# Performance work log

Hardware: AMD Instinct MI355X
Metric: run time of the kernel (lower is better)

Reference implementation:

```python
import jax, jax.numpy as jnp
import numpy as np

H, CH = 4, 16          # heads, hidden_features // heads
SLOPE = 0.2            # leaky_relu negative slope


def gat(x, W, a_src, a_dst):
    # x: (B, N, C); W: (hidden, C); a_src/a_dst: (H, CH)
    B, N, _ = x.shape
    h = (x @ W.T).reshape(B, N, H, CH)
    a1 = jnp.einsum('bnhc,hc->bnh', h, a_src)   # att_src scores
    a2 = jnp.einsum('bnhc,hc->bnh', h, a_dst)   # att_dst scores
    # torch: a1.unsqueeze(1) + a2.unsqueeze(2) -> (B, N, N, H)
    e = a1[:, None, :, :] + a2[:, :, None, :]
    e = jnp.transpose(e, (0, 3, 1, 2))          # (B, H, N, N)
    e = jnp.where(e >= 0, e, SLOPE * e)         # leaky_relu
    return jax.nn.softmax(e, axis=2)            # softmax over dim=2 as in torch


def pool(x, W1, b1, W2, b2):
    # diff-pool assignment: (B, N, K), then x' = S^T x -> (B, K, C)
    s = jax.nn.softmax(jax.nn.relu(x @ W1.T + b1) @ W2.T + b2, axis=-1)
    return jnp.einsum('bnk,bnc->bkc', s, x)


def fuse(att0, atts, lefts, rights):
    out = att0
    for a, l, r in zip(atts, lefts, rights):
        # left (H,J0,K) @ att (B,H,K,K) @ right (H,K,J0), broadcast over batch
        out = out + jnp.einsum('hjk,bhkl,hlm->bhjm', l, a, r)
    return out


def setup_inputs() -> dict:
    key = jax.random.key(0)
    ks = iter(jax.random.split(key, 40))
    n = lambda shape, s=0.1: jax.random.normal(next(ks), shape, dtype=jnp.float32) * s
    inp = {
        'src': n((64, 64, 64, 25), 1.0),
        'gat_lin': n((6, 64, 64)), 'gat_asrc': n((6, 4, 16)), 'gat_adst': n((6, 4, 16)),
        'sp0_W1': n((64, 64)), 'sp0_b1': jnp.zeros((64,), jnp.float32),
        'sp0_W2': n((12, 64)), 'sp0_b2': jnp.zeros((12,), jnp.float32),
        'sp1_W1': n((64, 64)), 'sp1_b1': jnp.zeros((64,), jnp.float32),
        'sp1_W2': n((5, 64)), 'sp1_b2': jnp.zeros((5,), jnp.float32),
        'tp0_W1': n((64, 64)), 'tp0_b1': jnp.zeros((64,), jnp.float32),
        'tp0_W2': n((32, 64)), 'tp0_b2': jnp.zeros((32,), jnp.float32),
        'tp1_W1': n((64, 64)), 'tp1_b1': jnp.zeros((64,), jnp.float32),
        'tp1_W2': n((12, 64)), 'tp1_b2': jnp.zeros((12,), jnp.float32),
        'sl0': n((4, 25, 12)), 'sr0': n((4, 12, 25)),
        'sl1': n((4, 25, 5)), 'sr1': n((4, 5, 25)),
        'tl0': n((4, 64, 32)), 'tr0': n((4, 32, 64)),
        'tl1': n((4, 64, 12)), 'tr1': n((4, 12, 64)),
    }
    return inp


def reference(src, gat_lin, gat_asrc, gat_adst,
              sp0_W1, sp0_b1, sp0_W2, sp0_b2, sp1_W1, sp1_b1, sp1_W2, sp1_b2,
              tp0_W1, tp0_b1, tp0_W2, tp0_b2, tp1_W1, tp1_b1, tp1_W2, tp1_b2,
              sl0, sr0, sl1, sr1, tl0, tr0, tl1, tr1):
    B, C, T, J = src.shape
    # ---- spatial branch: attention over joints per (batch, frame) ----
    xs = jnp.transpose(src, (0, 2, 3, 1)).reshape(B * T, J, C)
    a_s0 = gat(xs, gat_lin[0], gat_asrc[0], gat_adst[0])            # (BT,H,25,25)
    xs1 = pool(xs, sp0_W1, sp0_b1, sp0_W2, sp0_b2)                  # (BT,12,C)
    a_s1 = gat(xs1, gat_lin[1], gat_asrc[1], gat_adst[1])           # (BT,H,12,12)
    xs2 = pool(xs1, sp1_W1, sp1_b1, sp1_W2, sp1_b2)                 # (BT,5,C)
    a_s2 = gat(xs2, gat_lin[2], gat_asrc[2], gat_adst[2])           # (BT,H,5,5)
    s_fused = fuse(a_s0, [a_s1, a_s2], [sl0, sl1], [sr0, sr1])
    # ---- temporal branch: attention over frames per (batch, joint) ----
    xt = jnp.transpose(src, (0, 3, 2, 1)).reshape(B * J, T, C)
    a_t0 = gat(xt, gat_lin[3], gat_asrc[3], gat_adst[3])            # (BJ,H,64,64)
    xt1 = pool(xt, tp0_W1, tp0_b1, tp0_W2, tp0_b2)                  # (BJ,32,C)
    a_t1 = gat(xt1, gat_lin[4], gat_asrc[4], gat_adst[4])
    xt2 = pool(xt1, tp1_W1, tp1_b1, tp1_W2, tp1_b2)                 # (BJ,12,C)
    a_t2 = gat(xt2, gat_lin[5], gat_asrc[5], gat_adst[5])
    t_fused = fuse(a_t0, [a_t1, a_t2], [tl0, tl1], [tr0, tr1])
    return (s_fused.reshape(B, T, H, J, J), t_fused.reshape(B, J, H, T, T))
```

## Files before the change

### kernel.cpp

```cpp
#include <hip/hip_runtime.h>

#define DEVINL __device__ __forceinline__

DEVINL float leaky(float v) { return v >= 0.f ? v : 0.2f * v; }

typedef float v4f __attribute__((ext_vector_type(4)));

DEVINL void nt_store4(float* p, float4 v) {
    v4f q = {v.x, v.y, v.z, v.w};
    __builtin_nontemporal_store(q, (v4f*)p);
}

__global__ void wprep_kernel(const float* __restrict__ lin,
                             const float* __restrict__ asrc,
                             const float* __restrict__ adst,
                             float* __restrict__ w_out) {
    int idx = blockIdx.x * blockDim.x + threadIdx.x;
    if (idx >= 6 * 4 * 64) return;
    int c = idx & 63;
    int h = (idx >> 6) & 3;
    int k = idx >> 8;
    const float* L = lin + k * 64 * 64;
    float s1 = 0.f, s2 = 0.f;
    for (int e = 0; e < 16; ++e) {
        float w = L[(h * 16 + e) * 64 + c];
        s1 += w * asrc[(k * 4 + h) * 16 + e];
        s2 += w * adst[(k * 4 + h) * 16 + e];
    }
    w_out[(k * 2 + 0) * 256 + h * 64 + c] = s1;
    w_out[(k * 2 + 1) * 256 + h * 64 + c] = s2;
}

__global__ void wtrans_kernel(const float* __restrict__ s0, const float* __restrict__ s1,
                              const float* __restrict__ t0, const float* __restrict__ t1,
                              const float* __restrict__ s0w2, const float* __restrict__ s1w2,
                              const float* __restrict__ t0w2, const float* __restrict__ t1w2,
                              float* __restrict__ o) {
    int idx = blockIdx.x * 256 + threadIdx.x;
    if (idx < 16384) {
        int m = idx >> 12, r = idx & 4095, c = r >> 6, d = r & 63;
        const float* src = (m == 0) ? s0 : (m == 1) ? s1 : (m == 2) ? t0 : t1;
        o[idx] = src[d * 64 + c];
    } else if (idx < 16384 + 768) {
        int j = idx - 16384, c = j / 12, k = j - 12 * c;
        o[idx] = s0w2[k * 64 + c];
    } else if (idx < 17152 + 512) {
        int j = idx - 17152, c = j >> 3, k = j & 7;
        o[idx] = (k < 5) ? s1w2[k * 64 + c] : 0.f;
    } else if (idx < 17664 + 2048) {
        int j = idx - 17664, c = j >> 5, k = j & 31;
        o[idx] = t0w2[k * 64 + c];
    } else if (idx < 19712 + 768) {
        int j = idx - 19712, c = j / 12, k = j - 12 * c;
        o[idx] = t1w2[k * 64 + c];
    }
}

__global__ void xs_kernel(const float* __restrict__ src, float* __restrict__ xs) {
    int g = blockIdx.x;
    int b = g >> 6, t = g & 63;
    __shared__ float tile[64][26];
    const float* sp = src + b * 102400 + t * 25;
    for (int idx = threadIdx.x; idx < 64 * 25; idx += blockDim.x) {
        int c = idx / 25, j = idx - c * 25;
        tile[c][j] = sp[c * 1600 + j];
    }
    __syncthreads();
    float* op = xs + g * 25 * 64;
    for (int idx = threadIdx.x; idx < 25 * 64; idx += blockDim.x) {
        int j = idx >> 6, c = idx & 63;
        op[idx] = tile[c][j];
    }
}

__global__ void xt_kernel(const float* __restrict__ src, float* __restrict__ xt) {
    int g = blockIdx.x;
    int b = g / 25, j = g - b * 25;
    __shared__ float tile[64][65];
    const float* sp = src + b * 102400 + j;
    for (int idx = threadIdx.x; idx < 64 * 64; idx += blockDim.x) {
        int c = idx >> 6, t = idx & 63;
        tile[c][t] = sp[c * 1600 + t * 25];
    }
    __syncthreads();
    float* op = xt + g * 64 * 64;
    for (int idx = threadIdx.x; idx < 64 * 64; idx += blockDim.x) {
        int t = idx >> 6, c = idx & 63;
        op[idx] = tile[c][t];
    }
}

template <int N>
__global__ __launch_bounds__(256) void gat_kernel(
    const float* __restrict__ x,
    const float* __restrict__ w,
    float* __restrict__ att) {
    int g = blockIdx.x;
    const int tid = threadIdx.x;
    __shared__ float xlT[64][N + 1];
    __shared__ float wl[512];
    __shared__ float a1s[4 * N], a2s[4 * N];
    __shared__ float mxs[4];
    __shared__ float mjs[4 * N], invs[4 * N];
    const float* xp = x + (size_t)g * N * 64;
    for (int idx = tid; idx < N * 64; idx += 256) {
        int n = idx >> 6, c = idx & 63;
        xlT[c][n] = xp[idx];
    }
    for (int idx = tid; idx < 512; idx += 256) wl[idx] = w[idx];
    __syncthreads();
    for (int idx = tid; idx < 8 * N; idx += 256) {
        int n = idx % N;
        int hh = (idx / N) & 3;
        int sd = idx / (4 * N);
        const float* wp = wl + sd * 256 + hh * 64;
        float acc = 0.f;
        #pragma unroll 8
        for (int c = 0; c < 64; ++c) acc += xlT[c][n] * wp[c];
        (sd == 0 ? a1s : a2s)[hh * N + n] = acc;
    }
    __syncthreads();
    if (tid < 4) {
        float m = -1e30f;
        for (int i = 0; i < N; ++i) m = fmaxf(m, a2s[tid * N + i]);
        mxs[tid] = m;
    }
    __syncthreads();
    for (int idx = tid; idx < 4 * N; idx += 256) {
        int hh = idx / N;
        float aj = a1s[idx];
        float mj = leaky(aj + mxs[hh]);
        float ssum = 0.f;
        for (int i = 0; i < N; ++i) ssum += __expf(leaky(aj + a2s[hh * N + i]) - mj);
        mjs[idx] = mj;
        invs[idx] = 1.f / ssum;
    }
    __syncthreads();
    float* ob = att + (size_t)g * 4 * N * N;
    if constexpr ((N % 4) == 0) {
        constexpr int NF4 = N / 4;
        for (int idx = tid; idx < 4 * N * NF4; idx += 256) {
            int row = idx / NF4;
            int j0 = (idx - row * NF4) * 4;
            int hh = row / N;
            float4 q1 = *(const float4*)&a1s[hh * N + j0];
            float4 qm = *(const float4*)&mjs[hh * N + j0];
            float4 qv = *(const float4*)&invs[hh * N + j0];
            float a2i = a2s[row];
            float a1v[4] = {q1.x, q1.y, q1.z, q1.w};
            float mv[4] = {qm.x, qm.y, qm.z, qm.w};
            float iv[4] = {qv.x, qv.y, qv.z, qv.w};
            float r[4];
            #pragma unroll
            for (int c = 0; c < 4; ++c) {
                float e = a1v[c] + a2i;
                e = e >= 0.f ? e : 0.2f * e;
                r[c] = __expf(e - mv[c]) * iv[c];
            }
            *(float4*)&ob[row * N + j0] = make_float4(r[0], r[1], r[2], r[3]);
        }
    } else {
        for (int idx = tid; idx < 4 * N * N; idx += 256) {
            int hh = idx / (N * N), rem = idx - hh * N * N;
            int i = rem / N, j = rem - i * N;
            float e = a1s[hh * N + j] + a2s[hh * N + i];
            e = e >= 0.f ? e : 0.2f * e;
            ob[idx] = __expf(e - mjs[hh * N + j]) * invs[hh * N + j];
        }
    }
}

template <int N, int K, int KP>
__global__ __launch_bounds__(256, 3) void pool_kernel(
    const float* __restrict__ x,
    const float* __restrict__ W1T,
    const float* __restrict__ b1,
    const float* __restrict__ W2T,
    const float* __restrict__ b2,
    float* __restrict__ xo) {
    constexpr int NP = (N + 3) & ~3;
    constexpr int LDN = NP + 1;
    __shared__ float xlT[64 * LDN];
    __shared__ float yT[64 * LDN];
    __shared__ float sT[KP * LDN];
    const int g = blockIdx.x, tid = threadIdx.x;
    const float* xp = x + (size_t)g * N * 64;
    for (int i4 = tid; i4 < N * 16; i4 += 256) {
        int n = i4 >> 4, c0 = (i4 & 15) << 2;
        float4 v = ((const float4*)xp)[i4];
        xlT[(c0 + 0) * LDN + n] = v.x;
        xlT[(c0 + 1) * LDN + n] = v.y;
        xlT[(c0 + 2) * LDN + n] = v.z;
        xlT[(c0 + 3) * LDN + n] = v.w;
    }
    if constexpr (NP > N) {
        for (int i = tid; i < 64 * (NP - N); i += 256) {
            int c = i / (NP - N), n = N + i % (NP - N);
            xlT[c * LDN + n] = 0.f;
        }
    }
    __syncthreads();
    constexpr int T1 = (NP / 4) * 16;
    if (tid < T1) {
        int d0 = (tid & 15) << 2, n0 = (tid >> 4) << 2;
        float acc[4][4] = {};
        #pragma unroll 4
        for (int c = 0; c < 64; ++c) {
            float4 w4 = *(const float4*)(W1T + c * 64 + d0);
            float wv[4] = {w4.x, w4.y, w4.z, w4.w};
            float xv[4];
            #pragma unroll
            for (int r = 0; r < 4; ++r) xv[r] = xlT[c * LDN + n0 + r];
            #pragma unroll
            for (int r = 0; r < 4; ++r)
                #pragma unroll
                for (int cc = 0; cc < 4; ++cc) acc[r][cc] += xv[r] * wv[cc];
        }
        float4 b4 = *(const float4*)(b1 + d0);
        float bb[4] = {b4.x, b4.y, b4.z, b4.w};
        #pragma unroll
        for (int r = 0; r < 4; ++r)
            #pragma unroll
            for (int cc = 0; cc < 4; ++cc)
                yT[(d0 + cc) * LDN + n0 + r] = fmaxf(acc[r][cc] + bb[cc], 0.f);
    }
    __syncthreads();
    constexpr int KG4 = KP / 4;
    constexpr int T2 = (NP / 4) * KG4;
    if (tid < T2) {
        int k0 = (tid % KG4) << 2, n0 = (tid / KG4) << 2;
        float acc[4][4] = {};
        #pragma unroll 4
        for (int d = 0; d < 64; ++d) {
            float4 w4 = *(const float4*)(W2T + d * KP + k0);
            float wv[4] = {w4.x, w4.y, w4.z, w4.w};
            float yv[4];
            #pragma unroll
            for (int r = 0; r < 4; ++r) yv[r] = yT[d * LDN + n0 + r];
            #pragma unroll
            for (int r = 0; r < 4; ++r)
                #pragma unroll
                for (int cc = 0; cc < 4; ++cc) acc[r][cc] += yv[r] * wv[cc];
        }
        #pragma unroll
        for (int cc = 0; cc < 4; ++cc) {
            int k = k0 + cc;
            float bb = (k < K) ? b2[k] : 0.f;
            #pragma unroll
            for (int r = 0; r < 4; ++r)
                sT[k * LDN + n0 + r] = (k < K) ? (acc[r][cc] + bb) : -1e30f;
        }
    }
    __syncthreads();
    if (tid < NP) {
        float m = -1e30f;
        #pragma unroll
        for (int k = 0; k < KP; ++k) m = fmaxf(m, sT[k * LDN + tid]);
        float sum = 0.f;
        float e[KP];
        #pragma unroll
        for (int k = 0; k < KP; ++k) { e[k] = __expf(sT[k * LDN + tid] - m); sum += e[k]; }
        float inv = 1.f / sum;
        #pragma unroll
        for (int k = 0; k < KP; ++k) sT[k * LDN + tid] = e[k] * inv;
    }
    __syncthreads();
    constexpr int KG2 = (K + 1) / 2;
    constexpr int T3 = KG2 * 16;
    if (tid < T3) {
        int k0 = (tid % KG2) * 2, c0 = (tid / KG2) * 4;
        float acc0[4] = {}, acc1[4] = {};
        #pragma unroll 4
        for (int n = 0; n < N; ++n) {
            float sv0 = sT[k0 * LDN + n];
            float sv1 = sT[(k0 + 1) * LDN + n];
            float xv[4];
            #pragma unroll
            for (int j = 0; j < 4; ++j) xv[j] = xlT[(c0 + j) * LDN + n];
            #pragma unroll
            for (int j = 0; j < 4; ++j) { acc0[j] += sv0 * xv[j]; acc1[j] += sv1 * xv[j]; }
        }
        float* op = xo + (size_t)g * K * 64;
        *(float4*)&op[k0 * 64 + c0] = make_float4(acc0[0], acc0[1], acc0[2], acc0[3]);
        if (k0 + 1 < K)
            *(float4*)&op[(k0 + 1) * 64 + c0] = make_float4(acc1[0], acc1[1], acc1[2], acc1[3]);
    }
}

__global__ __launch_bounds__(256, 5) void gatfuse_t(
    const float* __restrict__ x,
    const float* __restrict__ w,
    const float* __restrict__ A1g,
    const float* __restrict__ L1,
    const float* __restrict__ R1,
    const float* __restrict__ A2g,
    const float* __restrict__ L2,
    const float* __restrict__ R2,
    float* __restrict__ out)
{
    const int bid = blockIdx.x;
    const int g = (bid & 7) | ((bid >> 5) << 3);
    const int h = (bid >> 3) & 3;
    const int tid = threadIdx.x;
    __shared__ float t1T[32 * 64];
    __shared__ float r1l[32 * 64];
    __shared__ float t2T[12 * 64];
    __shared__ float r2l[12 * 64];
    __shared__ float A1T[32 * 36];
    __shared__ float A2T[12 * 13];
    __shared__ float a1s[64], a2s[64], mjs[64], invs[64];

    if (tid < 128) {
        int t = tid & 63, sd = tid >> 6;
        const float4* xr = (const float4*)(x + (size_t)g * 4096 + t * 64);
        const float* wv = w + sd * 256 + h * 64;
        float acc = 0.f;
        #pragma unroll
        for (int q = 0; q < 16; ++q) {
            float4 xv = xr[q];
            acc += xv.x * wv[q * 4] + xv.y * wv[q * 4 + 1] +
                   xv.z * wv[q * 4 + 2] + xv.w * wv[q * 4 + 3];
        }
        (sd == 0 ? a1s : a2s)[t] = acc;
    } else {
        int u = tid - 128;
        const float* a1p = A1g + (size_t)(g * 4 + h) * 1024;
        #pragma unroll
        for (int q = 0; q < 8; ++q) {
            int idx = q * 128 + u;
            A1T[(idx & 31) * 36 + (idx >> 5)] = a1p[idx];
        }
        const float* a2p = A2g + (size_t)(g * 4 + h) * 144;
        for (int idx = u; idx < 144; idx += 128) {
            int k = idx / 12, l = idx - k * 12;
            A2T[l * 13 + k] = a2p[idx];
        }
        const float4* r1p = (const float4*)(R1 + h * 2048);
        #pragma unroll
        for (int q = 0; q < 4; ++q) ((float4*)r1l)[q * 128 + u] = r1p[q * 128 + u];
        const float4* r2p = (const float4*)(R2 + h * 768);
        for (int idx = u; idx < 192; idx += 128) ((float4*)r2l)[idx] = r2p[idx];
    }
    __syncthreads();

    if (tid < 64) {
        float mx = a2s[0];
        for (int i = 1; i < 64; ++i) mx = fmaxf(mx, a2s[i]);
        float aj = a1s[tid];
        float mj = leaky(aj + mx);
        float ssum = 0.f;
        for (int i = 0; i < 64; ++i) ssum += __expf(leaky(aj + a2s[i]) - mj);
        mjs[tid] = mj;
        invs[tid] = 1.f / ssum;
    }
    {
        int j = tid & 63, l0 = (tid >> 6) * 8;
        float lj[32];
        const float4* lp = (const float4*)(L1 + (h * 64 + j) * 32);
        #pragma unroll
        for (int q = 0; q < 8; ++q) {
            float4 v = lp[q];
            lj[q * 4] = v.x; lj[q * 4 + 1] = v.y; lj[q * 4 + 2] = v.z; lj[q * 4 + 3] = v.w;
        }
        for (int l = l0; l < l0 + 8; ++l) {
            const float* ar = &A1T[l * 36];
            float acc = 0.f;
            #pragma unroll
            for (int k = 0; k < 32; k += 4) {
                float4 av = *(const float4*)&ar[k];
                acc += lj[k] * av.x + lj[k + 1] * av.y + lj[k + 2] * av.z + lj[k + 3] * av.w;
            }
            t1T[l * 64 + j] = acc;
        }
    }
    {
        int j = tid & 63, lb = (tid >> 6) * 3;
        float lj2[12];
        const float* lp2 = L2 + (h * 64 + j) * 12;
        #pragma unroll
        for (int k = 0; k < 12; ++k) lj2[k] = lp2[k];
        for (int l = lb; l < lb + 3; ++l) {
            const float* ar = &A2T[l * 13];
            float acc = 0.f;
            #pragma unroll
            for (int k = 0; k < 12; ++k) acc += lj2[k] * ar[k];
            t2T[l * 64 + j] = acc;
        }
    }
    __syncthreads();

    const int i0 = (tid >> 4) << 2, m0 = (tid & 15) << 2;
    float acc[4][4];
    {
        float4 q1 = *(const float4*)&a1s[m0];
        float4 qm = *(const float4*)&mjs[m0];
        float4 qv = *(const float4*)&invs[m0];
        float4 q2 = *(const float4*)&a2s[i0];
        float am[4] = {q1.x, q1.y, q1.z, q1.w};
        float mv[4] = {qm.x, qm.y, qm.z, qm.w};
        float iv[4] = {qv.x, qv.y, qv.z, qv.w};
        float ai[4] = {q2.x, q2.y, q2.z, q2.w};
        #pragma unroll
        for (int r = 0; r < 4; ++r)
            #pragma unroll
            for (int c = 0; c < 4; ++c) {
                float e = am[c] + ai[r];
                e = e >= 0.f ? e : 0.2f * e;
                acc[r][c] = __expf(e - mv[c]) * iv[c];
            }
    }
    #pragma unroll 8
    for (int l = 0; l < 32; ++l) {
        float4 t4 = *(const float4*)&t1T[l * 64 + i0];
        float4 r4 = *(const float4*)&r1l[l * 64 + m0];
        float tv[4] = {t4.x, t4.y, t4.z, t4.w};
        float rv[4] = {r4.x, r4.y, r4.z, r4.w};
        #pragma unroll
        for (int r = 0; r < 4; ++r)
            #pragma unroll
            for (int c = 0; c < 4; ++c) acc[r][c] += tv[r] * rv[c];
    }
    #pragma unroll 4
    for (int l = 0; l < 12; ++l) {
        float4 t4 = *(const float4*)&t2T[l * 64 + i0];
        float4 r4 = *(const float4*)&r2l[l * 64 + m0];
        float tv[4] = {t4.x, t4.y, t4.z, t4.w};
        float rv[4] = {r4.x, r4.y, r4.z, r4.w};
        #pragma unroll
        for (int r = 0; r < 4; ++r)
            #pragma unroll
            for (int c = 0; c < 4; ++c) acc[r][c] += tv[r] * rv[c];
    }
    float* op = out + (size_t)(g * 4 + h) * 4096;
    #pragma unroll
    for (int r = 0; r < 4; ++r)
        nt_store4(&op[(i0 + r) * 64 + m0],
                  make_float4(acc[r][0], acc[r][1], acc[r][2], acc[r][3]));
}

__global__ __launch_bounds__(256) void gatfuse_s(
    const float* __restrict__ x,
    const float* __restrict__ w,
    const float* __restrict__ A1g,
    const float* __restrict__ L1,
    const float* __restrict__ R1,
    const float* __restrict__ A2g,
    const float* __restrict__ L2,
    const float* __restrict__ R2,
    float* __restrict__ out)
{
    const int g = blockIdx.x;
    const int tid = threadIdx.x;
    const int h = tid >> 6, t = tid & 63;
    __shared__ float xl[25 * 68];
    __shared__ float A1T[4][12 * 12];
    __shared__ float A2T[4][5 * 5];
    __shared__ float t1l[4][25 * 12];
    __shared__ float t2l[4][25 * 5];
    __shared__ float r1l[4][12 * 25];
    __shared__ float r2l[4][5 * 25];
    __shared__ float a1s[4][25], a2s[4][25], mjs[4][32], invs[4][32];

    const float* xp = x + (size_t)g * 1600;
    for (int idx = tid; idx < 1600; idx += 256) {
        int n = idx >> 6, c = idx & 63;
        xl[n * 68 + c] = xp[idx];
    }
    const float* a1p = A1g + (size_t)(g * 4 + h) * 144;
    for (int idx = t; idx < 144; idx += 64) {
        int k = idx / 12, l = idx - k * 12;
        A1T[h][l * 12 + k] = a1p[idx];
    }
    const float* a2p = A2g + (size_t)(g * 4 + h) * 25;
    if (t < 25) {
        int k = t / 5, l = t - 5 * (t / 5);
        A2T[h][l * 5 + k] = a2p[t];
    }
    for (int idx = t; idx < 300; idx += 64) r1l[h][idx] = R1[h * 300 + idx];
    for (int idx = t; idx < 125; idx += 64) r2l[h][idx] = R2[h * 125 + idx];
    __syncthreads();

    if (t < 25) {
        const float* ws_ = w + h * 64;
        const float* wd_ = w + 256 + h * 64;
        const float* xr = &xl[t * 68];
        float s1 = 0.f, s2 = 0.f;
        #pragma unroll
        for (int c = 0; c < 64; c += 4) {
            float4 xv = *(const float4*)&xr[c];
            s1 += xv.x * ws_[c] + xv.y * ws_[c + 1] + xv.z * ws_[c + 2] + xv.w * ws_[c + 3];
            s2 += xv.x * wd_[c] + xv.y * wd_[c + 1] + xv.z * wd_[c + 2] + xv.w * wd_[c + 3];
        }
        a1s[h][t] = s1;
        a2s[h][t] = s2;
    }
    __syncthreads();

    if (t < 25) {
        float mx = a2s[h][0];
        for (int i = 1; i < 25; ++i) mx = fmaxf(mx, a2s[h][i]);
        float aj = a1s[h][t];
        float mj = leaky(aj + mx);
        float ssum = 0.f;
        for (int i = 0; i < 25; ++i) ssum += __expf(leaky(aj + a2s[h][i]) - mj);
        mjs[h][t] = mj;
        invs[h][t] = 1.f / ssum;
        float lj[12];
        const float* lp = L1 + (h * 25 + t) * 12;
        #pragma unroll
        for (int k = 0; k < 12; ++k) lj[k] = lp[k];
        #pragma unroll
        for (int l = 0; l < 12; ++l) {
            const float* ar = &A1T[h][l * 12];
            float acc = 0.f;
            #pragma unroll
            for (int k = 0; k < 12; ++k) acc += lj[k] * ar[k];
            t1l[h][t * 12 + l] = acc;
        }
        float lj2[5];
        const float* lp2 = L2 + (h * 25 + t) * 5;
        #pragma unroll
        for (int k = 0; k < 5; ++k) lj2[k] = lp2[k];
        #pragma unroll
        for (int l = 0; l < 5; ++l) {
            const float* ar = &A2T[h][l * 5];
            float acc = 0.f;
            #pragma unroll
            for (int k = 0; k < 5; ++k) acc += lj2[k] * ar[k];
            t2l[h][t * 5 + l] = acc;
        }
    }
    __syncthreads();

    float* op = out + (size_t)(g * 4 + h) * 625;
    for (int idx = t; idx < 625; idx += 64) {
        int i = idx / 25, m = idx - i * 25;
        float e = a1s[h][m] + a2s[h][i];
        e = e >= 0.f ? e : 0.2f * e;
        float val = __expf(e - mjs[h][m]) * invs[h][m];
        const float* t1r = &t1l[h][i * 12];
        const float* r1c = &r1l[h][m];
        #pragma unroll
        for (int l = 0; l < 12; ++l) val += t1r[l] * r1c[l * 25];
        const float* t2r = &t2l[h][i * 5];
        const float* r2c = &r2l[h][m];
        #pragma unroll
        for (int l = 0; l < 5; ++l) val += t2r[l] * r2c[l * 25];
        __builtin_nontemporal_store(val, &op[idx]);
    }
}

extern "C" void kernel_launch(void* const* d_in, const int* in_sizes, int n_in,
                              void* d_out, int out_size, void* d_ws, size_t ws_size,
                              hipStream_t stream) {
    const float* src    = (const float*)d_in[0];
    const float* lin    = (const float*)d_in[1];
    const float* asrc   = (const float*)d_in[2];
    const float* adst   = (const float*)d_in[3];
    const float* sp0_W1 = (const float*)d_in[4];
    const float* sp0_b1 = (const float*)d_in[5];
    const float* sp0_W2 = (const float*)d_in[6];
    const float* sp0_b2 = (const float*)d_in[7];
    const float* sp1_W1 = (const float*)d_in[8];
    const float* sp1_b1 = (const float*)d_in[9];
    const float* sp1_W2 = (const float*)d_in[10];
    const float* sp1_b2 = (const float*)d_in[11];
    const float* tp0_W1 = (const float*)d_in[12];
    const float* tp0_b1 = (const float*)d_in[13];
    const float* tp0_W2 = (const float*)d_in[14];
    const float* tp0_b2 = (const float*)d_in[15];
    const float* tp1_W1 = (const float*)d_in[16];
    const float* tp1_b1 = (const float*)d_in[17];
    const float* tp1_W2 = (const float*)d_in[18];
    const float* tp1_b2 = (const float*)d_in[19];
    const float* sl0    = (const float*)d_in[20];
    const float* sr0    = (const float*)d_in[21];
    const float* sl1    = (const float*)d_in[22];
    const float* sr1    = (const float*)d_in[23];
    const float* tl0    = (const float*)d_in[24];
    const float* tr0    = (const float*)d_in[25];
    const float* tl1    = (const float*)d_in[26];
    const float* tr1    = (const float*)d_in[27];

    float* out_s = (float*)d_out;
    float* out_t = out_s + 10240000;

    float* ws   = (float*)d_ws;
    float* wbuf = ws;
    float* wT   = ws + 4096;
    float* region = ws + 24576;

    float* sp0_W1T = wT;
    float* sp1_W1T = wT + 4096;
    float* tp0_W1T = wT + 8192;
    float* tp1_W1T = wT + 12288;
    float* sp0_W2T = wT + 16384;
    float* sp1_W2T = wT + 17152;
    float* tp0_W2T = wT + 17664;
    float* tp1_W2T = wT + 19712;

    float* xs  = region;
    float* xs1 = xs + 6553600;
    float* xs2 = xs1 + 3145728;
    float* as1 = xs2 + 1310720;
    float* as2 = as1 + 2359296;
    float* xt  = region;
    float* xt1 = xt + 6553600;
    float* xt2 = xt1 + 3276800;
    float* at1 = xt2 + 1228800;
    float* at2 = at1 + 6553600;

    wprep_kernel<<<6, 256, 0, stream>>>(lin, asrc, adst, wbuf);
    wtrans_kernel<<<80, 256, 0, stream>>>(sp0_W1, sp1_W1, tp0_W1, tp1_W1,
                                          sp0_W2, sp1_W2, tp0_W2, tp1_W2, wT);

    xs_kernel<<<4096, 256, 0, stream>>>(src, xs);
    pool_kernel<25, 12, 12><<<4096, 256, 0, stream>>>(xs, sp0_W1T, sp0_b1, sp0_W2T, sp0_b2, xs1);
    gat_kernel<12><<<4096, 256, 0, stream>>>(xs1, wbuf + 1 * 512, as1);
    pool_kernel<12, 5, 8><<<4096, 256, 0, stream>>>(xs1, sp1_W1T, sp1_b1, sp1_W2T, sp1_b2, xs2);
    gat_kernel<5><<<4096, 256, 0, stream>>>(xs2, wbuf + 2 * 512, as2);
    gatfuse_s<<<4096, 256, 0, stream>>>(xs, wbuf + 0 * 512, as1, sl0, sr0, as2, sl1, sr1, out_s);

    xt_kernel<<<1600, 256, 0, stream>>>(src, xt);
    pool_kernel<64, 32, 32><<<1600, 256, 0, stream>>>(xt, tp0_W1T, tp0_b1, tp0_W2T, tp0_b2, xt1);
    gat_kernel<32><<<1600, 256, 0, stream>>>(xt1, wbuf + 4 * 512, at1);
    pool_kernel<32, 12, 12><<<1600, 256, 0, stream>>>(xt1, tp1_W1T, tp1_b1, tp1_W2T, tp1_b2, xt2);
    gat_kernel<12><<<1600, 256, 0, stream>>>(xt2, wbuf + 5 * 512, at2);
    gatfuse_t<<<6400, 256, 0, stream>>>(xt, wbuf + 3 * 512, at1, tl0, tr0, at2, tl1, tr1, out_t);
}
```

Baseline: 355.7 us.

## Rebalance pool small-N/K work mapping and shrink gatfuse_t shared memory via bf16

```diff
diff --git a/kernel.cpp b/kernel.cpp
--- a/kernel.cpp
+++ b/kernel.cpp
@@ -10,6 +10,14 @@
     v4f q = {v.x, v.y, v.z, v.w};
     __builtin_nontemporal_store(q, (v4f*)p);
 }
+
+DEVINL unsigned short f2bf(float f) {
+    unsigned int u = __float_as_uint(f);
+    unsigned int r = (u + 0x7FFFu + ((u >> 16) & 1u)) >> 16;
+    return (unsigned short)r;
+}
+DEVINL float bflo(unsigned int u) { return __uint_as_float(u << 16); }
+DEVINL float bfhi(unsigned int u) { return __uint_as_float(u & 0xFFFF0000u); }
 
 __global__ void wprep_kernel(const float* __restrict__ lin,
                              const float* __restrict__ asrc,
@@ -200,59 +208,97 @@
         }
     }
     __syncthreads();
-    constexpr int T1 = (NP / 4) * 16;
-    if (tid < T1) {
-        int d0 = (tid & 15) << 2, n0 = (tid >> 4) << 2;
-        float acc[4][4] = {};
-        #pragma unroll 4
-        for (int c = 0; c < 64; ++c) {
-            float4 w4 = *(const float4*)(W1T + c * 64 + d0);
-            float wv[4] = {w4.x, w4.y, w4.z, w4.w};
-            float xv[4];
-            #pragma unroll
-            for (int r = 0; r < 4; ++r) xv[r] = xlT[c * LDN + n0 + r];
+    if constexpr (NP <= 32) {
+        constexpr int T1 = (NP / 2) * 16;
+        if (tid < T1) {
+            int d0 = (tid & 15) << 2, n0 = (tid >> 4) << 1;
+            float acc[2][4] = {};
+            #pragma unroll 4
+            for (int c = 0; c < 64; ++c) {
+                float4 w4 = *(const float4*)(W1T + c * 64 + d0);
+                float wv[4] = {w4.x, w4.y, w4.z, w4.w};
+                float x0 = xlT[c * LDN + n0];
+                float x1 = xlT[c * LDN + n0 + 1];
+                #pragma unroll
+                for (int cc = 0; cc < 4; ++cc) {
+                    acc[0][cc] += x0 * wv[cc];
+                    acc[1][cc] += x1 * wv[cc];
+                }
+            }
+            float4 b4 = *(const float4*)(b1 + d0);
+            float bb[4] = {b4.x, b4.y, b4.z, b4.w};
+            #pragma unroll
+            for (int r = 0; r < 2; ++r)
+                #pragma unroll
+                for (int cc = 0; cc < 4; ++cc)
+                    yT[(d0 + cc) * LDN + n0 + r] = fmaxf(acc[r][cc] + bb[cc], 0.f);
+        }
+    } else {
+        constexpr int T1 = (NP / 4) * 16;
+        if (tid < T1) {
+            int d0 = (tid & 15) << 2, n0 = (tid >> 4) << 2;
+            float acc[4][4] = {};
+            #pragma unroll 4
+            for (int c = 0; c < 64; ++c) {
+                float4 w4 = *(const float4*)(W1T + c * 64 + d0);
+                float wv[4] = {w4.x, w4.y, w4.z, w4.w};
+                float xv[4];
+                #pragma unroll
+                for (int r = 0; r < 4; ++r) xv[r] = xlT[c * LDN + n0 + r];
+                #pragma unroll
+                for (int r = 0; r < 4; ++r)
+                    #pragma unroll
+                    for (int cc = 0; cc < 4; ++cc) acc[r][cc] += xv[r] * wv[cc];
+            }
+            float4 b4 = *(const float4*)(b1 + d0);
+            float bb[4] = {b4.x, b4.y, b4.z, b4.w};
             #pragma unroll
             for (int r = 0; r < 4; ++r)
                 #pragma unroll
-                for (int cc = 0; cc < 4; ++cc) acc[r][cc] += xv[r] * wv[cc];
-        }
-        float4 b4 = *(const float4*)(b1 + d0);
-        float bb[4] = {b4.x, b4.y, b4.z, b4.w};
-        #pragma unroll
-        for (int r = 0; r < 4; ++r)
-            #pragma unroll
-            for (int cc = 0; cc < 4; ++cc)
-                yT[(d0 + cc) * LDN + n0 + r] = fmaxf(acc[r][cc] + bb[cc], 0.f);
-    }
-    __syncthreads();
-    constexpr int KG4 = KP / 4;
-    constexpr int T2 = (NP / 4) * KG4;
-    if (tid < T2) {
-        int k0 = (tid % KG4) << 2, n0 = (tid / KG4) << 2;
-        float acc[4][4] = {};
-        #pragma unroll 4
-        for (int d = 0; d < 64; ++d) {
-            float4 w4 = *(const float4*)(W2T + d * KP + k0);
-            float wv[4] = {w4.x, w4.y, w4.z, w4.w};
-            float yv[4];
-            #pragma unroll
-            for (int r = 0; r < 4; ++r) yv[r] = yT[d * LDN + n0 + r];
-            #pragma unroll
-            for (int r = 0; r < 4; ++r)
-                #pragma unroll
-                for (int cc = 0; cc < 4; ++cc) acc[r][cc] += yv[r] * wv[cc];
-        }
-        #pragma unroll
-        for (int cc = 0; cc < 4; ++cc) {
-            int k = k0 + cc;
-            float bb = (k < K) ? b2[k] : 0.f;
-            #pragma unroll
-            for (int r = 0; r < 4; ++r)
-                sT[k * LDN + n0 + r] = (k < K) ? (acc[r][cc] + bb) : -1e30f;
-        }
-    }
-    __syncthreads();
-    if (tid < NP) {
+                for (int cc = 0; cc < 4; ++cc)
+                    yT[(d0 + cc) * LDN + n0 + r] = fmaxf(acc[r][cc] + bb[cc], 0.f);
+        }
+    }
+    __syncthreads();
+    if constexpr (KP <= 12) {
+        for (int p = tid; p < N * KP; p += 256) {
+            int n = p / KP, k = p - n * KP;
+            float acc = 0.f;
+            #pragma unroll 8
+            for (int d = 0; d < 64; ++d)
+                acc += yT[d * LDN + n] * W2T[d * KP + k];
+            sT[k * LDN + n] = (k < K) ? (acc + b2[k]) : -1e30f;
+        }
+    } else {
+        constexpr int KG4 = KP / 4;
+        constexpr int T2 = (NP / 4) * KG4;
+        if (tid < T2) {
+            int k0 = (tid % KG4) << 2, n0 = (tid / KG4) << 2;
+            float acc[4][4] = {};
+            #pragma unroll 4
+            for (int d = 0; d < 64; ++d) {
+                float4 w4 = *(const float4*)(W2T + d * KP + k0);
+                float wv[4] = {w4.x, w4.y, w4.z, w4.w};
+                float yv[4];
+                #pragma unroll
+                for (int r = 0; r < 4; ++r) yv[r] = yT[d * LDN + n0 + r];
+                #pragma unroll
+                for (int r = 0; r < 4; ++r)
+                    #pragma unroll
+                    for (int cc = 0; cc < 4; ++cc) acc[r][cc] += yv[r] * wv[cc];
+            }
+            #pragma unroll
+            for (int cc = 0; cc < 4; ++cc) {
+                int k = k0 + cc;
+                float bb = (k < K) ? b2[k] : 0.f;
+                #pragma unroll
+                for (int r = 0; r < 4; ++r)
+                    sT[k * LDN + n0 + r] = (k < K) ? (acc[r][cc] + bb) : -1e30f;
+            }
+        }
+    }
+    __syncthreads();
+    if (tid < N) {
         float m = -1e30f;
         #pragma unroll
         for (int k = 0; k < KP; ++k) m = fmaxf(m, sT[k * LDN + tid]);
@@ -287,7 +333,7 @@
     }
 }
 
-__global__ __launch_bounds__(256, 5) void gatfuse_t(
+__global__ __launch_bounds__(256, 6) void gatfuse_t(
     const float* __restrict__ x,
     const float* __restrict__ w,
     const float* __restrict__ A1g,
@@ -304,8 +350,8 @@
     const int tid = threadIdx.x;
     __shared__ float t1T[32 * 64];
     __shared__ float r1l[32 * 64];
-    __shared__ float t2T[12 * 64];
-    __shared__ float r2l[12 * 64];
+    __shared__ unsigned short t2Tb[12 * 64];
+    __shared__ unsigned short r2lb[12 * 64];
     __shared__ float A1T[32 * 36];
     __shared__ float A2T[12 * 13];
     __shared__ float a1s[64], a2s[64], mjs[64], invs[64];
@@ -338,8 +384,8 @@
         const float4* r1p = (const float4*)(R1 + h * 2048);
         #pragma unroll
         for (int q = 0; q < 4; ++q) ((float4*)r1l)[q * 128 + u] = r1p[q * 128 + u];
-        const float4* r2p = (const float4*)(R2 + h * 768);
-        for (int idx = u; idx < 192; idx += 128) ((float4*)r2l)[idx] = r2p[idx];
+        const float* r2p = R2 + h * 768;
+        for (int idx = u; idx < 768; idx += 128) r2lb[idx] = f2bf(r2p[idx]);
     }
     __syncthreads();
 
@@ -384,7 +430,7 @@
             float acc = 0.f;
             #pragma unroll
             for (int k = 0; k < 12; ++k) acc += lj2[k] * ar[k];
-            t2T[l * 64 + j] = acc;
+            t2Tb[l * 64 + j] = f2bf(acc);
         }
     }
     __syncthreads();
@@ -422,10 +468,10 @@
     }
     #pragma unroll 4
     for (int l = 0; l < 12; ++l) {
-        float4 t4 = *(const float4*)&t2T[l * 64 + i0];
-        float4 r4 = *(const float4*)&r2l[l * 64 + m0];
-        float tv[4] = {t4.x, t4.y, t4.z, t4.w};
-        float rv[4] = {r4.x, r4.y, r4.z, r4.w};
+        uint2 tp = *(const uint2*)&t2Tb[l * 64 + i0];
+        uint2 rp = *(const uint2*)&r2lb[l * 64 + m0];
+        float tv[4] = {bflo(tp.x), bfhi(tp.x), bflo(tp.y), bfhi(tp.y)};
+        float rv[4] = {bflo(rp.x), bfhi(rp.x), bflo(rp.y), bfhi(rp.y)};
         #pragma unroll
         for (int r = 0; r < 4; ++r)
             #pragma unroll
```

Measured after the change: 368.6 us. 1.04x slower.
